# Kernel tuning notes

Hardware: AMD Instinct MI355X
Metric: run time of the kernel (lower is better)

Reference implementation:

```python
import jax, jax.numpy as jnp
import numpy as np

HIDDEN = 256
EDGE_DIM = 16
HEADS = 8
HEAD_DIM = HIDDEN // HEADS
B, N = 4, 512


def setup_inputs() -> dict:
    key = jax.random.key(0)
    ks = jax.random.split(key, 16)
    s = 1.0 / np.sqrt(HIDDEN)
    se = 1.0 / np.sqrt(EDGE_DIM)
    return {
        "node_h": jax.random.normal(ks[0], (B, N, HIDDEN), jnp.float32),
        "edge_x": jax.random.normal(ks[1], (B, N, N, EDGE_DIM), jnp.float32),
        "edge_mask": jax.random.randint(ks[2], (B, N, N), 0, 2, jnp.int32),
        "Wq": jax.random.normal(ks[3], (HIDDEN, HIDDEN), jnp.float32) * s,
        "bq": jnp.zeros((HIDDEN,), jnp.float32),
        "Wk": jax.random.normal(ks[4], (HIDDEN, HIDDEN), jnp.float32) * s,
        "bk": jnp.zeros((HIDDEN,), jnp.float32),
        "Wv": jax.random.normal(ks[5], (HIDDEN, HIDDEN), jnp.float32) * s,
        "bv": jnp.zeros((HIDDEN,), jnp.float32),
        "We1": jax.random.normal(ks[6], (EDGE_DIM, HIDDEN), jnp.float32) * se,
        "be1": jnp.zeros((HIDDEN,), jnp.float32),
        "We2": jax.random.normal(ks[7], (HIDDEN, HEADS), jnp.float32) * s,
        "be2": jnp.zeros((HEADS,), jnp.float32),
        "Wo": jax.random.normal(ks[8], (HIDDEN, HIDDEN), jnp.float32) * s,
        "bo": jnp.zeros((HIDDEN,), jnp.float32),
        "ln_g": jnp.ones((HIDDEN,), jnp.float32),
        "ln_b": jnp.zeros((HIDDEN,), jnp.float32),
    }


def reference(node_h, edge_x, edge_mask, Wq, bq, Wk, bk, Wv, bv,
              We1, be1, We2, be2, Wo, bo, ln_g, ln_b):
    Bsz, Nn, _ = node_h.shape
    # projections -> [B, H, N, D]
    def heads(x):
        return x.reshape(Bsz, Nn, HEADS, HEAD_DIM).transpose(0, 2, 1, 3)
    q = heads(node_h @ Wq + bq)
    k = heads(node_h @ Wk + bk)
    v = heads(node_h @ Wv + bv)

    scores = jnp.einsum('bhid,bhjd->bhij', q, k) / np.sqrt(HEAD_DIM)
    scores = jax.nn.leaky_relu(scores, negative_slope=0.2)

    # edge bias MLP: [B,N,N,E] -> [B,N,N,H] -> [B,H,N,N]
    eb = jax.nn.relu(edge_x @ We1 + be1) @ We2 + be2
    scores = scores + eb.transpose(0, 3, 1, 2)

    valid = (edge_mask != 0) | jnp.eye(Nn, dtype=bool)[None]  # [B,N,N]
    scores = jnp.where(valid[:, None], scores, -1e9)

    attn = jax.nn.softmax(scores, axis=-1)
    out = jnp.einsum('bhij,bhjd->bhid', attn, v)
    out = out.transpose(0, 2, 1, 3).reshape(Bsz, Nn, HIDDEN)
    out = out @ Wo + bo

    x = node_h + out
    mu = jnp.mean(x, axis=-1, keepdims=True)
    var = jnp.var(x, axis=-1, keepdims=True)
    x = (x - mu) / jnp.sqrt(var + 1e-5) * ln_g + ln_b
    return jax.nn.relu(x), attn
```

## Files before the change

kernel.cpp:

```cpp
#include <hip/hip_runtime.h>

#define BATCH 4
#define NN 512
#define HID 256
#define EDIM 16
#define HEADS 8
#define HDIM 32

typedef __attribute__((ext_vector_type(8))) short bf16x8;
typedef __attribute__((ext_vector_type(4))) float f32x4;

__device__ inline unsigned short bf16_hi(float x){ return (unsigned short)(__float_as_uint(x)>>16); }
__device__ inline float bf16_f(unsigned short s){ return __uint_as_float(((unsigned)s)<<16); }
__device__ inline unsigned short bf16_rn(float x){
    unsigned u = __float_as_uint(x);
    unsigned r = u + 0x7FFFu + ((u>>16)&1u);
    return (unsigned short)(r>>16);
}
__device__ inline unsigned cvt_pk_bf16(float a, float b){
    unsigned d;
    asm("v_cvt_pk_bf16_f32 %0, %1, %2" : "=v"(d) : "v"(a), "v"(b));
    return d;
}
__device__ inline void hilo8(float4 A, float4 B, bf16x8& hi, bf16x8& lo){
    float xs[8] = {A.x,A.y,A.z,A.w,B.x,B.y,B.z,B.w};
    unsigned hu[4], lu[4];
#pragma unroll
    for (int p = 0; p < 4; ++p){
        unsigned u0 = __float_as_uint(xs[2*p]), u1 = __float_as_uint(xs[2*p+1]);
        float h0 = __uint_as_float(u0 & 0xFFFF0000u);
        float h1 = __uint_as_float(u1 & 0xFFFF0000u);
        hu[p] = (u0 >> 16) | (u1 & 0xFFFF0000u);
        lu[p] = cvt_pk_bf16(xs[2*p] - h0, xs[2*p+1] - h1);
    }
    int4 hv; hv.x = hu[0]; hv.y = hu[1]; hv.z = hu[2]; hv.w = hu[3];
    int4 lv; lv.x = lu[0]; lv.y = lu[1]; lv.z = lu[2]; lv.w = lu[3];
    hi = *(bf16x8*)&hv; lo = *(bf16x8*)&lv;
}

__global__ void k_pack(const float* __restrict__ We1, const float* __restrict__ be1,
                       const float* __restrict__ We2,
                       unsigned short* __restrict__ W1P, unsigned short* __restrict__ W2P) {
    int t = threadIdx.x;
#pragma unroll
    for (int rep = 0; rep < 4; ++rep) {
        int p = rep * 256 + t;
        int ut = p >> 6, lane = p & 63;
        int q = lane >> 4, r = lane & 15;
        int unit = ut * 16 + r;
#pragma unroll
        for (int j = 0; j < 8; ++j) {
            int k = q * 8 + j;
            unsigned short ov;
            if (k < 16) ov = bf16_hi(We1[k * HID + unit]);
            else if (k < 31) {
                float v = We1[(k - 16) * HID + unit];
                ov = bf16_rn(v - bf16_f(bf16_hi(v)));
            } else ov = bf16_rn(be1[unit]);
            W1P[p * 8 + j] = ov;
        }
    }
#pragma unroll
    for (int rep = 0; rep < 2; ++rep) {
        int p = rep * 256 + t;
        int kt = p >> 6, lane = p & 63;
        int q = lane >> 4, r = lane & 15;
#pragma unroll
        for (int jj = 0; jj < 8; ++jj) {
            int unit = kt * 32 + q * 8 + jj;
            W2P[p * 8 + jj] = (r < 8) ? bf16_rn(We2[unit * HEADS + r]) : (unsigned short)0;
        }
    }
}

__global__ __launch_bounds__(256) void k_qkv(
    const float* __restrict__ node_h,
    const float* __restrict__ Wq, const float* __restrict__ bq,
    const float* __restrict__ Wk, const float* __restrict__ bk,
    const float* __restrict__ Wv, const float* __restrict__ bv,
    float* __restrict__ q, float* __restrict__ k, float* __restrict__ vT) {
    int blk = blockIdx.x;
    int b = blk >> 7, i0 = (blk & 127) << 2;
    int t = threadIdx.x;
    __shared__ __align__(16) float s_h[4][HID];
#pragma unroll
    for (int u = 0; u < 4; ++u)
        s_h[u][t] = node_h[((size_t)b * NN + i0 + u) * HID + t];
    __syncthreads();
    float aq[4], ak[4], av[4];
    float bqv = bq[t], bkv = bk[t], bvv = bv[t];
#pragma unroll
    for (int u = 0; u < 4; ++u) { aq[u] = bqv; ak[u] = bkv; av[u] = bvv; }
#pragma unroll 4
    for (int rr = 0; rr < HID; ++rr) {
        float wq = Wq[rr * HID + t], wk = Wk[rr * HID + t], wv = Wv[rr * HID + t];
#pragma unroll
        for (int u = 0; u < 4; ++u) {
            float x = s_h[u][rr];
            aq[u] = fmaf(x, wq, aq[u]);
            ak[u] = fmaf(x, wk, ak[u]);
            av[u] = fmaf(x, wv, av[u]);
        }
    }
    int h = t >> 5, d = t & 31;
#pragma unroll
    for (int u = 0; u < 4; ++u) {
        size_t idx = ((size_t)(b * HEADS + h) * NN + i0 + u) * HDIM + d;
        q[idx] = aq[u]; k[idx] = ak[u];
        vT[((size_t)(b * HEADS + h) * HDIM + d) * NN + i0 + u] = av[u];
    }
}

__global__ __launch_bounds__(256, 3) void k_eb(
    const float* __restrict__ edge_x,
    const unsigned short* __restrict__ W1P, const unsigned short* __restrict__ W2P,
    const float* __restrict__ be2, float* __restrict__ eb) {
    int bid = blockIdx.x;
    int b = bid >> 9, i0 = ((bid >> 2) & 127) << 2, jq = bid & 3;
    int t = threadIdx.x;
    int w = t >> 6, lane = t & 63;
    int q2 = lane >> 4, r = lane & 15;

    bf16x8 W1Pr[16];
#pragma unroll
    for (int ut = 0; ut < 16; ++ut)
        W1Pr[ut] = *(const bf16x8*)(W1P + ((size_t)ut * 64 + lane) * 8);
    bf16x8 w2f[8];
#pragma unroll
    for (int kt = 0; kt < 8; ++kt)
        w2f[kt] = *(const bf16x8*)(W2P + ((size_t)kt * 64 + lane) * 8);
    float be2r = (r < 8) ? be2[r] : 0.f;

    size_t xbase = (((size_t)b * NN + i0 + w) * NN) * EDIM + (size_t)((q2 & 1) * 8);
    const f32x4 zero4 = {0.f, 0.f, 0.f, 0.f};
    for (int c = 0; c < 8; ++c) {
        int cc = jq * 8 + c;
        const float4* px = (const float4*)(edge_x + xbase + (size_t)(cc * 16 + r) * EDIM);
        float4 x0 = px[0], x1 = px[1];
        unsigned u0 = cvt_pk_bf16(x0.x, x0.y);
        unsigned u1 = cvt_pk_bf16(x0.z, x0.w);
        unsigned u2 = cvt_pk_bf16(x1.x, x1.y);
        unsigned u3 = cvt_pk_bf16(x1.z, x1.w);
        if (q2 == 3) u3 = (u3 & 0xFFFFu) | 0x3F800000u;
        int4 bxi; bxi.x = u0; bxi.y = u1; bxi.z = u2; bxi.w = u3;
        bf16x8 bx = *(bf16x8*)&bxi;

        f32x4 acc = {be2r, be2r, be2r, be2r};
#pragma unroll
        for (int qt = 0; qt < 4; ++qt) {
#pragma unroll
            for (int pr = 0; pr < 2; ++pr) {
                int ut0 = qt * 4 + pr * 2;
                f32x4 c0 = __builtin_amdgcn_mfma_f32_16x16x32_bf16(W1Pr[ut0],     bx, zero4, 0, 0, 0);
                f32x4 c1 = __builtin_amdgcn_mfma_f32_16x16x32_bf16(W1Pr[ut0 + 1], bx, zero4, 0, 0, 0);
                unsigned P0 = cvt_pk_bf16(fmaxf(c0[0], 0.f), fmaxf(c0[1], 0.f));
                unsigned P1 = cvt_pk_bf16(fmaxf(c0[2], 0.f), fmaxf(c0[3], 0.f));
                unsigned Q0 = cvt_pk_bf16(fmaxf(c1[0], 0.f), fmaxf(c1[1], 0.f));
                unsigned Q1 = cvt_pk_bf16(fmaxf(c1[2], 0.f), fmaxf(c1[3], 0.f));
                asm("v_permlane32_swap_b32 %0, %1" : "+v"(P0), "+v"(Q0));
                asm("v_permlane16_swap_b32 %0, %1" : "+v"(P0), "+v"(Q0));
                asm("v_permlane32_swap_b32 %0, %1" : "+v"(P1), "+v"(Q1));
                asm("v_permlane16_swap_b32 %0, %1" : "+v"(P1), "+v"(Q1));
                int4 ai; ai.x = (int)P0; ai.y = (int)P1; ai.z = (int)Q0; ai.w = (int)Q1;
                acc = __builtin_amdgcn_mfma_f32_16x16x32_bf16(*(bf16x8*)&ai, w2f[qt * 2 + pr], acc, 0, 0, 0);
            }
        }
        if (r < 8)
            *(f32x4*)(eb + (((size_t)(b * HEADS + r) * NN) + (i0 + w)) * NN + cc * 16 + q2 * 4) = acc;
    }
}

__global__ __launch_bounds__(256, 3) void k_attn2(
    const int* __restrict__ emask,
    const float* __restrict__ q, const float* __restrict__ k, const float* __restrict__ vT,
    float* attn, float* __restrict__ ao) {
    int bid = blockIdx.x;
    int b = bid >> 8, h = (bid >> 5) & 7, ic = bid & 31;
    int i0 = ic << 4;
    int t = threadIdx.x, w = t >> 6, lane = t & 63;
    int q2 = lane >> 4, r = lane & 15;
    size_t bh = (size_t)b * HEADS + h;

    __shared__ __align__(16) float s_sc[16][516];
    __shared__ __align__(16) unsigned short s_ab[16][520];
    __shared__ float s_out[2][16][33];

    bf16x8 qhi, qlo;
    {
        const float4* qp = (const float4*)(q + ((bh * NN) + i0 + r) * HDIM + q2 * 8);
        hilo8(qp[0], qp[1], qhi, qlo);
    }

    const float scale = 0.17677669529663687f;
    for (int c = 0; c < 8; ++c) {
        int jt = w * 8 + c;
        bf16x8 khi, klo;
        {
            const float4* kp = (const float4*)(k + (bh * NN + jt * 16 + r) * HDIM + q2 * 8);
            hilo8(kp[0], kp[1], khi, klo);
        }
        f32x4 cc = {0.f, 0.f, 0.f, 0.f};
        cc = __builtin_amdgcn_mfma_f32_16x16x32_bf16(qhi, khi, cc, 0, 0, 0);
        cc = __builtin_amdgcn_mfma_f32_16x16x32_bf16(qhi, klo, cc, 0, 0, 0);
        cc = __builtin_amdgcn_mfma_f32_16x16x32_bf16(qlo, khi, cc, 0, 0, 0);
        int j = jt * 16 + r;
#pragma unroll
        for (int reg = 0; reg < 4; ++reg) {
            int row = q2 * 4 + reg;
            int i = i0 + row;
            float s = cc[reg] * scale;
            s = s > 0.f ? s : 0.2f * s;
            s += attn[(bh * NN + i) * NN + j];
            bool valid = (emask[((size_t)b * NN + i) * NN + j] != 0) || (j == i);
            s_sc[row][j] = valid ? s : -1e9f;
        }
    }
    __syncthreads();

#pragma unroll
    for (int rr = 0; rr < 4; ++rr) {
        int row = w * 4 + rr;
        f32x4 v0 = *(f32x4*)&s_sc[row][lane * 8];
        f32x4 v1 = *(f32x4*)&s_sc[row][lane * 8 + 4];
        float mx = fmaxf(fmaxf(fmaxf(v0[0], v0[1]), fmaxf(v0[2], v0[3])),
                         fmaxf(fmaxf(v1[0], v1[1]), fmaxf(v1[2], v1[3])));
#pragma unroll
        for (int off = 32; off > 0; off >>= 1) mx = fmaxf(mx, __shfl_xor(mx, off));
        float e[8];
        e[0] = __expf(v0[0] - mx); e[1] = __expf(v0[1] - mx);
        e[2] = __expf(v0[2] - mx); e[3] = __expf(v0[3] - mx);
        e[4] = __expf(v1[0] - mx); e[5] = __expf(v1[1] - mx);
        e[6] = __expf(v1[2] - mx); e[7] = __expf(v1[3] - mx);
        float sum = ((e[0] + e[1]) + (e[2] + e[3])) + ((e[4] + e[5]) + (e[6] + e[7]));
#pragma unroll
        for (int off = 32; off > 0; off >>= 1) sum += __shfl_xor(sum, off);
        float inv = 1.f / sum;
#pragma unroll
        for (int l = 0; l < 8; ++l) e[l] *= inv;
        float* arow = attn + (bh * NN + i0 + row) * NN + lane * 8;
        float4 o0; o0.x = e[0]; o0.y = e[1]; o0.z = e[2]; o0.w = e[3];
        float4 o1; o1.x = e[4]; o1.y = e[5]; o1.z = e[6]; o1.w = e[7];
        *(float4*)(arow) = o0;
        *(float4*)(arow + 4) = o1;
        uint4 pk;
        pk.x = cvt_pk_bf16(e[0], e[1]); pk.y = cvt_pk_bf16(e[2], e[3]);
        pk.z = cvt_pk_bf16(e[4], e[5]); pk.w = cvt_pk_bf16(e[6], e[7]);
        *(uint4*)((char*)s_ab + row * 1040 + lane * 16) = pk;
    }
    __syncthreads();

    {
        int part = w >> 1, nh = w & 1;
        const float* vbase = vT + (bh * HDIM + nh * 16 + r) * NN;
        f32x4 acc = {0.f, 0.f, 0.f, 0.f};
        for (int kt = 0; kt < 16; ++kt) {
            bf16x8 af = *(bf16x8*)((char*)s_ab + r * 1040 + kt * 64 + q2 * 16);
            const float4* vp = (const float4*)(vbase + kt * 32 + q2 * 8);
            float4 x0 = vp[0], x1 = vp[1];
            float xs[8] = {x0.x, x0.y, x0.z, x0.w, x1.x, x1.y, x1.z, x1.w};
            bf16x8 bfg;
            if (part == 0) {
                unsigned hu[4];
#pragma unroll
                for (int p = 0; p < 4; ++p) {
                    unsigned a0 = __float_as_uint(xs[2*p]), a1 = __float_as_uint(xs[2*p+1]);
                    hu[p] = (a0 >> 16) | (a1 & 0xFFFF0000u);
                }
                int4 hv; hv.x = hu[0]; hv.y = hu[1]; hv.z = hu[2]; hv.w = hu[3];
                bfg = *(bf16x8*)&hv;
            } else {
                unsigned lu[4];
#pragma unroll
                for (int p = 0; p < 4; ++p) {
                    unsigned a0 = __float_as_uint(xs[2*p]), a1 = __float_as_uint(xs[2*p+1]);
                    float h0 = __uint_as_float(a0 & 0xFFFF0000u);
                    float h1 = __uint_as_float(a1 & 0xFFFF0000u);
                    lu[p] = cvt_pk_bf16(xs[2*p] - h0, xs[2*p+1] - h1);
                }
                int4 lv; lv.x = lu[0]; lv.y = lu[1]; lv.z = lu[2]; lv.w = lu[3];
                bfg = *(bf16x8*)&lv;
            }
            acc = __builtin_amdgcn_mfma_f32_16x16x32_bf16(af, bfg, acc, 0, 0, 0);
        }
#pragma unroll
        for (int reg = 0; reg < 4; ++reg)
            s_out[part][q2 * 4 + reg][nh * 16 + r] = acc[reg];
    }
    __syncthreads();

#pragma unroll
    for (int rep = 0; rep < 2; ++rep) {
        int idx = rep * 256 + t;
        int row = idx >> 5, d = idx & 31;
        ao[((size_t)b * NN + i0 + row) * HID + h * HDIM + d] =
            s_out[0][row][d] + s_out[1][row][d];
    }
}

__global__ __launch_bounds__(256) void k_final(
    const float* __restrict__ ao, const float* __restrict__ node_h,
    const float* __restrict__ Wo, const float* __restrict__ bo,
    const float* __restrict__ ln_g, const float* __restrict__ ln_b,
    float* __restrict__ out) {
    int blk = blockIdx.x;
    size_t bi0 = (size_t)blk * 4;
    int t = threadIdx.x;
    __shared__ __align__(16) float s_a[4][HID];
    __shared__ float s_red[4][4][2];
#pragma unroll
    for (int u = 0; u < 4; ++u)
        s_a[u][t] = ao[(bi0 + u) * HID + t];
    __syncthreads();
    float bov = bo[t];
    float o[4];
#pragma unroll
    for (int u = 0; u < 4; ++u) o[u] = bov;
#pragma unroll 4
    for (int rr = 0; rr < HID; ++rr) {
        float wo = Wo[rr * HID + t];
#pragma unroll
        for (int u = 0; u < 4; ++u) o[u] = fmaf(s_a[u][rr], wo, o[u]);
    }
    float g = ln_g[t], bb = ln_b[t];
    int wave = t >> 6, ln = t & 63;
    float x[4];
#pragma unroll
    for (int u = 0; u < 4; ++u) {
        x[u] = node_h[(bi0 + u) * HID + t] + o[u];
        float s1 = x[u], s2 = x[u] * x[u];
#pragma unroll
        for (int off = 32; off > 0; off >>= 1) { s1 += __shfl_xor(s1, off); s2 += __shfl_xor(s2, off); }
        if (ln == 0) { s_red[u][wave][0] = s1; s_red[u][wave][1] = s2; }
    }
    __syncthreads();
#pragma unroll
    for (int u = 0; u < 4; ++u) {
        float s1 = s_red[u][0][0] + s_red[u][1][0] + s_red[u][2][0] + s_red[u][3][0];
        float s2 = s_red[u][0][1] + s_red[u][1][1] + s_red[u][2][1] + s_red[u][3][1];
        float mean = s1 * (1.f / HID);
        float var = s2 * (1.f / HID) - mean * mean;
        float inv = rsqrtf(var + 1e-5f);
        float y = (x[u] - mean) * inv * g + bb;
        out[(bi0 + u) * HID + t] = fmaxf(y, 0.f);
    }
}

extern "C" void kernel_launch(void* const* d_in, const int* in_sizes, int n_in,
                              void* d_out, int out_size, void* d_ws, size_t ws_size,
                              hipStream_t stream) {
    const float* node_h = (const float*)d_in[0];
    const float* edge_x = (const float*)d_in[1];
    const int*   emask  = (const int*)d_in[2];
    const float* Wq = (const float*)d_in[3];
    const float* bq = (const float*)d_in[4];
    const float* Wk = (const float*)d_in[5];
    const float* bk = (const float*)d_in[6];
    const float* Wv = (const float*)d_in[7];
    const float* bv = (const float*)d_in[8];
    const float* We1 = (const float*)d_in[9];
    const float* be1 = (const float*)d_in[10];
    const float* We2 = (const float*)d_in[11];
    const float* be2 = (const float*)d_in[12];
    const float* Wo = (const float*)d_in[13];
    const float* bo = (const float*)d_in[14];
    const float* ln_g = (const float*)d_in[15];
    const float* ln_b = (const float*)d_in[16];

    float* out_x  = (float*)d_out;
    float* out_at = (float*)d_out + (size_t)BATCH * NN * HID;

    float* ws = (float*)d_ws;
    float* q    = ws;
    float* kbuf = ws + 524288;
    float* vT   = ws + 1048576;
    float* ao   = ws + 1572864;
    unsigned short* W1P = (unsigned short*)(ws + 2097152);
    unsigned short* W2P = W1P + 8192;

    const int NBI = BATCH * NN;

    hipLaunchKernelGGL(k_pack, dim3(1), dim3(256), 0, stream, We1, be1, We2, W1P, W2P);
    hipLaunchKernelGGL(k_qkv, dim3(NBI / 4), dim3(256), 0, stream,
                       node_h, Wq, bq, Wk, bk, Wv, bv, q, kbuf, vT);
    hipLaunchKernelGGL(k_eb, dim3(2048), dim3(256), 0, stream,
                       edge_x, W1P, W2P, be2, out_at);
    hipLaunchKernelGGL(k_attn2, dim3(1024), dim3(256), 0, stream,
                       emask, q, kbuf, vT, out_at, ao);
    hipLaunchKernelGGL(k_final, dim3(NBI / 4), dim3(256), 0, stream,
                       ao, node_h, Wo, bo, ln_g, ln_b, out_x);
}
```

Before: 148.5 us.

## Stage edge-MLP weights in LDS and batch four column chunks per iteration

The edge-bias kernel now copies the W1/W2 MFMA fragments into shared memory once per block and reads them per k-step, instead of holding 24 bf16x8 weight registers per thread. Each iteration processes four 16-column chunks at once, loading all their edge_x values up front. It also splits accumulation into two independent accumulator chains, which gives more independent MFMAs to hide latency and overlaps global loads. The cost is 24KB of LDS per block plus LDS reads inside the inner loop, which may limit occupancy at 3 blocks per CU, and more accumulator registers.

After: 147.6 us (median of 2 runs). About the same (-0.6%).

```diff
diff --git a/kernel.cpp b/kernel.cpp
--- a/kernel.cpp
+++ b/kernel.cpp
@@ -121,38 +121,63 @@
     int w = t >> 6, lane = t & 63;
     int q2 = lane >> 4, r = lane & 15;
 
-    bf16x8 W1Pr[16];
-#pragma unroll
-    for (int ut = 0; ut < 16; ++ut)
-        W1Pr[ut] = *(const bf16x8*)(W1P + ((size_t)ut * 64 + lane) * 8);
-    bf16x8 w2f[8];
-#pragma unroll
-    for (int kt = 0; kt < 8; ++kt)
-        w2f[kt] = *(const bf16x8*)(W2P + ((size_t)kt * 64 + lane) * 8);
+    __shared__ __align__(16) unsigned short sW1[8192];
+    __shared__ __align__(16) unsigned short sW2[4096];
+
+    {
+        const float4* s1 = (const float4*)W1P;
+        float4* d1 = (float4*)sW1;
+#pragma unroll
+        for (int rep = 0; rep < 4; ++rep) d1[rep * 256 + t] = s1[rep * 256 + t];
+        const float4* s2 = (const float4*)W2P;
+        float4* d2 = (float4*)sW2;
+#pragma unroll
+        for (int rep = 0; rep < 2; ++rep) d2[rep * 256 + t] = s2[rep * 256 + t];
+    }
+    __syncthreads();
+
     float be2r = (r < 8) ? be2[r] : 0.f;
+    const char* wb1 = (const char*)sW1 + lane * 16;
+    const char* wb2 = (const char*)sW2 + lane * 16;
 
     size_t xbase = (((size_t)b * NN + i0 + w) * NN) * EDIM + (size_t)((q2 & 1) * 8);
     const f32x4 zero4 = {0.f, 0.f, 0.f, 0.f};
-    for (int c = 0; c < 8; ++c) {
-        int cc = jq * 8 + c;
-        const float4* px = (const float4*)(edge_x + xbase + (size_t)(cc * 16 + r) * EDIM);
-        float4 x0 = px[0], x1 = px[1];
-        unsigned u0 = cvt_pk_bf16(x0.x, x0.y);
-        unsigned u1 = cvt_pk_bf16(x0.z, x0.w);
-        unsigned u2 = cvt_pk_bf16(x1.x, x1.y);
-        unsigned u3 = cvt_pk_bf16(x1.z, x1.w);
-        if (q2 == 3) u3 = (u3 & 0xFFFFu) | 0x3F800000u;
-        int4 bxi; bxi.x = u0; bxi.y = u1; bxi.z = u2; bxi.w = u3;
-        bf16x8 bx = *(bf16x8*)&bxi;
-
-        f32x4 acc = {be2r, be2r, be2r, be2r};
-#pragma unroll
-        for (int qt = 0; qt < 4; ++qt) {
-#pragma unroll
-            for (int pr = 0; pr < 2; ++pr) {
-                int ut0 = qt * 4 + pr * 2;
-                f32x4 c0 = __builtin_amdgcn_mfma_f32_16x16x32_bf16(W1Pr[ut0],     bx, zero4, 0, 0, 0);
-                f32x4 c1 = __builtin_amdgcn_mfma_f32_16x16x32_bf16(W1Pr[ut0 + 1], bx, zero4, 0, 0, 0);
+
+    for (int sc = 0; sc < 2; ++sc) {
+        int cc0 = jq * 8 + sc * 4;
+        float4 xv[8];
+#pragma unroll
+        for (int x = 0; x < 4; ++x) {
+            const float4* px = (const float4*)(edge_x + xbase + (size_t)((cc0 + x) * 16 + r) * EDIM);
+            xv[2 * x]     = px[0];
+            xv[2 * x + 1] = px[1];
+        }
+        bf16x8 bx[4];
+#pragma unroll
+        for (int x = 0; x < 4; ++x) {
+            unsigned u0 = cvt_pk_bf16(xv[2*x].x, xv[2*x].y);
+            unsigned u1 = cvt_pk_bf16(xv[2*x].z, xv[2*x].w);
+            unsigned u2 = cvt_pk_bf16(xv[2*x+1].x, xv[2*x+1].y);
+            unsigned u3 = cvt_pk_bf16(xv[2*x+1].z, xv[2*x+1].w);
+            if (q2 == 3) u3 = (u3 & 0xFFFFu) | 0x3F800000u;
+            int4 bxi; bxi.x = u0; bxi.y = u1; bxi.z = u2; bxi.w = u3;
+            bx[x] = *(bf16x8*)&bxi;
+        }
+        f32x4 acc0[4], acc1[4];
+#pragma unroll
+        for (int x = 0; x < 4; ++x) {
+            acc0[x] = (f32x4){be2r, be2r, be2r, be2r};
+            acc1[x] = zero4;
+        }
+#pragma unroll
+        for (int ktp = 0; ktp < 8; ++ktp) {
+            bf16x8 wa = *(const bf16x8*)(wb1 + (2 * ktp) * 1024);
+            bf16x8 wb = *(const bf16x8*)(wb1 + (2 * ktp + 1) * 1024);
+            bf16x8 w2 = *(const bf16x8*)(wb2 + ktp * 1024);
+#pragma unroll
+            for (int x = 0; x < 4; ++x) {
+                f32x4 c0 = __builtin_amdgcn_mfma_f32_16x16x32_bf16(wa, bx[x], zero4, 0, 0, 0);
+                f32x4 c1 = __builtin_amdgcn_mfma_f32_16x16x32_bf16(wb, bx[x], zero4, 0, 0, 0);
                 unsigned P0 = cvt_pk_bf16(fmaxf(c0[0], 0.f), fmaxf(c0[1], 0.f));
                 unsigned P1 = cvt_pk_bf16(fmaxf(c0[2], 0.f), fmaxf(c0[3], 0.f));
                 unsigned Q0 = cvt_pk_bf16(fmaxf(c1[0], 0.f), fmaxf(c1[1], 0.f));
@@ -162,11 +187,19 @@
                 asm("v_permlane32_swap_b32 %0, %1" : "+v"(P1), "+v"(Q1));
                 asm("v_permlane16_swap_b32 %0, %1" : "+v"(P1), "+v"(Q1));
                 int4 ai; ai.x = (int)P0; ai.y = (int)P1; ai.z = (int)Q0; ai.w = (int)Q1;
-                acc = __builtin_amdgcn_mfma_f32_16x16x32_bf16(*(bf16x8*)&ai, w2f[qt * 2 + pr], acc, 0, 0, 0);
+                if (ktp & 1)
+                    acc1[x] = __builtin_amdgcn_mfma_f32_16x16x32_bf16(*(bf16x8*)&ai, w2, acc1[x], 0, 0, 0);
+                else
+                    acc0[x] = __builtin_amdgcn_mfma_f32_16x16x32_bf16(*(bf16x8*)&ai, w2, acc0[x], 0, 0, 0);
             }
         }
-        if (r < 8)
-            *(f32x4*)(eb + (((size_t)(b * HEADS + r) * NN) + (i0 + w)) * NN + cc * 16 + q2 * 4) = acc;
+        if (r < 8) {
+#pragma unroll
+            for (int x = 0; x < 4; ++x) {
+                f32x4 a = acc0[x] + acc1[x];
+                *(f32x4*)(eb + (((size_t)(b * HEADS + r) * NN) + (i0 + w)) * NN + (cc0 + x) * 16 + q2 * 4) = a;
+            }
+        }
     }
 }
 
```
